# Optimization experiments

Hardware: AMD Instinct MI355X
Metric: run time of the kernel (lower is better)

## Reference

```python
import jax, jax.numpy as jnp
import numpy as np

HC = 64                 # half_context
PAD = HC + 3            # padding_idx row of positional table
NEG = 1.0e12            # additive mask constant from the torch code


def setup_inputs() -> dict:
    key = jax.random.key(0)
    ks = jax.random.split(key, 7)
    B, S, D, C = 32, 2048, 1024, 256
    embeds = jax.random.normal(ks[0], (B, S, D), dtype=jnp.float32)
    embeds_mask = jnp.ones((B, S), dtype=jnp.float32)
    latent = jax.random.normal(ks[1], (C, D), dtype=jnp.float32)
    att_diag = jax.random.normal(ks[2], (D,), dtype=jnp.float32)
    tok_diag = jax.random.normal(ks[3], (D,), dtype=jnp.float32)
    pos_table = jax.random.normal(ks[4], (2 * HC + 4, D), dtype=jnp.float32)
    pos_table = pos_table.at[PAD].set(0.0)  # padding_idx row is zeros
    tok_mult = jnp.ones((1,), dtype=jnp.float32)
    rel_pos_ids = jax.random.randint(ks[5], (B, S), 0, HC + 4, dtype=jnp.int32)
    return {
        "embeds": embeds,
        "embeds_mask": embeds_mask,
        "latent": latent,
        "att_diag": att_diag,
        "tok_diag": tok_diag,
        "pos_table": pos_table,
        "tok_mult": tok_mult,
        "rel_pos_ids": rel_pos_ids,
    }


def reference(embeds, embeds_mask, latent, att_diag, tok_diag, pos_table, tok_mult, rel_pos_ids):
    # positional-embedding gather and merge (dropouts are identity in eval)
    absolute_pos = rel_pos_ids + HC                       # [B,S]
    pos_embeds = pos_table[absolute_pos]                  # [B,S,D]
    merged = tok_mult[0] * embeds + pos_embeds            # [B,S,D]
    # entity-token attention scores: (latent * diag) @ merged^T
    scores = jnp.einsum('cd,bsd->bcs', latent * att_diag, merged)  # [B,C,S]
    m = embeds_mask[:, None, :]                           # [B,1,S]
    scores = scores * m + (m - 1.0) * NEG                 # mask-add
    top = jnp.max(scores, axis=1)                         # max over classes -> [B,S]
    att_probs = jax.nn.softmax(top, axis=1)               # softmax over tokens
    # weighted sum of (embeds * tok_diag) by attention probs -> [B,D]
    ctx_vecs = jnp.einsum('bsd,d,bs->bd', embeds, tok_diag, att_probs)
    return ctx_vecs
```

## Files before the change

### kernel.cpp

```cpp
#include <hip/hip_runtime.h>
#include <hip/hip_bf16.h>


#define HC 64
#define NEGV 1000000000000.0f

constexpr int Bb = 32, Ss = 2048, Dd = 1024, Cc = 256;
constexpr int NKC = 32;
constexpr int CT = Cc / 16;
constexpr int NBLK = 16;

typedef _Float16 f16x8 __attribute__((ext_vector_type(8)));
typedef float    f32x4 __attribute__((ext_vector_type(4)));

__global__ __launch_bounds__(256) void k_prep_w(
    const float* __restrict__ latent, const float* __restrict__ att_diag,
    _Float16* __restrict__ whi)
{
    const int idx = blockIdx.x * 256 + threadIdx.x;
    const int c = idx >> 10, k = idx & 1023;
    const float wv = latent[idx] * att_diag[k];
    const int kc = k >> 5, g = (k >> 3) & 3, i = k & 7;
    const int lane = (c & 15) + 16 * g, ct = c >> 4;
    whi[(size_t)kc * 8192 + (size_t)ct * 512 + lane * 8 + i] = (_Float16)wv;
}

__global__ __launch_bounds__(256, 2) void k_scores_mfma(
    const float* __restrict__ embeds,
    const float* __restrict__ mask,
    const float* __restrict__ pos_table,
    const float* __restrict__ tok_mult,
    const int*   __restrict__ rel_ids,
    const _Float16* __restrict__ whi,
    float* __restrict__ partial,
    float* __restrict__ mblk,
    float* __restrict__ zblk)
{
    __shared__ _Float16 sbufW[2][8192];
    __shared__ float    sbufE[2][4096];
    __shared__ float l_sh[128];
    __shared__ float w_sh[128];
    __shared__ float red2[2], zred[2];

    const int t  = threadIdx.x;
    const int wv = t >> 6;
    const int l  = t & 63;
    const int lr = l & 15;
    const int lg = l >> 4;

    const int b   = blockIdx.x >> 4;
    const int blk = blockIdx.x & 15;
    const int s0  = blk * 128;

    const float tm = tok_mult[0];

    const float* prow[2];
    #pragma unroll
    for (int st = 0; st < 2; st++) {
        const int tok = s0 + wv * 32 + st * 16 + lr;
        prow[st] = pos_table + (size_t)(rel_ids[b * Ss + tok] + HC) * Dd;
    }

    f32x4 acc[CT][2];
    #pragma unroll
    for (int ct = 0; ct < CT; ct++)
        #pragma unroll
        for (int st = 0; st < 2; st++) acc[ct][st] = (f32x4){0.f, 0.f, 0.f, 0.f};

    f32x4 p0[2], p1[2];
    auto loadP = [&](int kc) {
        const int k0 = kc * 32 + lg * 8;
        #pragma unroll
        for (int st = 0; st < 2; st++) {
            p0[st] = *(const f32x4*)(prow[st] + k0);
            p1[st] = *(const f32x4*)(prow[st] + k0 + 4);
        }
    };

    auto stageW = [&](int kc, _Float16* dst) {
        const _Float16* src = whi + (size_t)kc * 8192;
        #pragma unroll
        for (int i = 0; i < 4; i++) {
            const int off = (i * 4 + wv) << 9;
            __builtin_amdgcn_global_load_lds(
                (const __attribute__((address_space(1))) void*)(src + off + l * 8),
                (__attribute__((address_space(3))) void*)(dst + off),
                16, 0, 0);
        }
    };

    auto stageE = [&](int kc, float* dst) {
        const float* ebase = embeds + ((size_t)b * Ss + s0) * Dd + kc * 32;
        #pragma unroll
        for (int i = 0; i < 4; i++) {
            const int jbase = i * 256 + wv * 64;
            const int j = jbase + l;
            const int row = j >> 3, u = j & 7;
            const float* src = ebase + (size_t)row * Dd + ((u ^ (row & 7)) << 2);
            __builtin_amdgcn_global_load_lds(
                (const __attribute__((address_space(1))) void*)src,
                (__attribute__((address_space(3))) void*)(dst + jbase * 4),
                16, 0, 0);
        }
    };

    stageW(0, sbufW[0]);
    stageE(0, sbufE[0]);
    loadP(0);
    asm volatile("s_waitcnt vmcnt(4)" ::: "memory");
    __builtin_amdgcn_s_barrier();

    int cur = 0;
    for (int kc = 0; kc < NKC; kc++) {
        if (kc + 1 < NKC) {
            stageW(kc + 1, sbufW[cur ^ 1]);
            stageE(kc + 1, sbufE[cur ^ 1]);
        }

        f16x8 bh[2], bl[2];
        {
            const float* es = sbufE[cur];
            #pragma unroll
            for (int st = 0; st < 2; st++) {
                const int row = wv * 32 + st * 16 + lr;
                const int sw  = row & 7;
                const f32x4 x0 = *(const f32x4*)(es + row * 32 + (((lg << 1)    ) ^ sw) * 4);
                const f32x4 x1 = *(const f32x4*)(es + row * 32 + (((lg << 1) | 1) ^ sw) * 4);
                float e[8], p[8];
                *(f32x4*)&e[0] = x0;     *(f32x4*)&e[4] = x1;
                *(f32x4*)&p[0] = p0[st]; *(f32x4*)&p[4] = p1[st];
                #pragma unroll
                for (int i = 0; i < 8; i++) {
                    const float x = fmaf(tm, e[i], p[i]);
                    const _Float16 h = (_Float16)x;
                    bh[st][i] = h;
                    bl[st][i] = (_Float16)(x - (float)h);
                }
            }
        }
        if (kc + 1 < NKC) loadP(kc + 1);

        const _Float16* base = sbufW[cur];
        #pragma unroll
        for (int ct = 0; ct < CT; ct++) {
            const f16x8 ah = *(const f16x8*)(base + ct * 512 + l * 8);
            #pragma unroll
            for (int st = 0; st < 2; st++) {
                acc[ct][st] = __builtin_amdgcn_mfma_f32_16x16x32_f16(ah, bh[st], acc[ct][st], 0, 0, 0);
                acc[ct][st] = __builtin_amdgcn_mfma_f32_16x16x32_f16(ah, bl[st], acc[ct][st], 0, 0, 0);
            }
        }
        if (kc + 1 < NKC) { asm volatile("s_waitcnt vmcnt(4)" ::: "memory"); }
        else              { asm volatile("s_waitcnt vmcnt(0)" ::: "memory"); }
        __builtin_amdgcn_s_barrier();
        cur ^= 1;
    }

    #pragma unroll
    for (int st = 0; st < 2; st++) {
        float mx = acc[0][st][0];
        #pragma unroll
        for (int ct = 0; ct < CT; ct++)
            #pragma unroll
            for (int r = 0; r < 4; r++) mx = fmaxf(mx, acc[ct][st][r]);
        mx = fmaxf(mx, __shfl_xor(mx, 16));
        mx = fmaxf(mx, __shfl_xor(mx, 32));
        if (lg == 0) {
            const int si = wv * 32 + st * 16 + lr;
            const int s  = s0 + si;
            const float mk = mask[b * Ss + s];
            l_sh[si] = mx * mk + (mk - 1.0f) * NEGV;
        }
    }
    __syncthreads();

    if (t < 128) {
        float v = l_sh[t];
        #pragma unroll
        for (int o = 32; o >= 1; o >>= 1) v = fmaxf(v, __shfl_xor(v, o));
        if ((t & 63) == 0) red2[t >> 6] = v;
    }
    __syncthreads();
    const float Mb = fmaxf(red2[0], red2[1]);
    if (t < 128) w_sh[t] = expf(l_sh[t] - Mb);
    __syncthreads();
    if (t < 128) {
        float z = w_sh[t];
        #pragma unroll
        for (int o = 32; o >= 1; o >>= 1) z += __shfl_xor(z, o);
        if ((t & 63) == 0) zred[t >> 6] = z;
    }
    __syncthreads();

    {
        const float* eb = embeds + ((size_t)b * Ss + s0) * Dd + t * 4;
        f32x4 ca = (f32x4){0.f, 0.f, 0.f, 0.f};
        #pragma unroll 8
        for (int s = 0; s < 128; s++) {
            const float wgt = w_sh[s];
            const f32x4 ev = *(const f32x4*)(eb + (size_t)s * Dd);
            ca[0] = fmaf(wgt, ev[0], ca[0]);
            ca[1] = fmaf(wgt, ev[1], ca[1]);
            ca[2] = fmaf(wgt, ev[2], ca[2]);
            ca[3] = fmaf(wgt, ev[3], ca[3]);
        }
        *(f32x4*)(partial + ((size_t)(b * NBLK + blk)) * Dd + t * 4) = ca;
        if (t == 0) {
            mblk[b * NBLK + blk] = Mb;
            zblk[b * NBLK + blk] = zred[0] + zred[1];
        }
    }
}

__global__ __launch_bounds__(256) void k_finish(
    const float* __restrict__ mblk, const float* __restrict__ zblk,
    const float* __restrict__ partial, const float* __restrict__ tok_diag,
    float* __restrict__ out)
{
    __shared__ float cf[NBLK];
    const int b  = blockIdx.x >> 2;
    const int dq = blockIdx.x & 3;
    const int t  = threadIdx.x;

    if (t < 64) {
        const float mv = (t < NBLK) ? mblk[b * NBLK + t] : -3.4e38f;
        float M = mv;
        #pragma unroll
        for (int o = 32; o >= 1; o >>= 1) M = fmaxf(M, __shfl_xor(M, o));
        const float zv = (t < NBLK) ? zblk[b * NBLK + t] * expf(mv - M) : 0.f;
        float Z = zv;
        #pragma unroll
        for (int o = 32; o >= 1; o >>= 1) Z += __shfl_xor(Z, o);
        if (t < NBLK) cf[t] = expf(mv - M) / Z;
    }
    __syncthreads();

    const int d = dq * 256 + t;
    float a = 0.f;
    #pragma unroll
    for (int j = 0; j < NBLK; j++)
        a = fmaf(cf[j], partial[((size_t)(b * NBLK + j)) * Dd + d], a);
    out[(size_t)b * Dd + d] = a * tok_diag[d];
}

extern "C" void kernel_launch(void* const* d_in, const int* in_sizes, int n_in,
                              void* d_out, int out_size, void* d_ws, size_t ws_size,
                              hipStream_t stream) {
    const float* embeds    = (const float*)d_in[0];
    const float* mask      = (const float*)d_in[1];
    const float* latent    = (const float*)d_in[2];
    const float* att_diag  = (const float*)d_in[3];
    const float* tok_diag  = (const float*)d_in[4];
    const float* pos_table = (const float*)d_in[5];
    const float* tok_mult  = (const float*)d_in[6];
    const int*   rel_ids   = (const int*)d_in[7];
    float* out = (float*)d_out;

    char* ws = (char*)d_ws;
    _Float16* whi    = (_Float16*)(ws);
    float*    partial= (float*)(ws + 524288);
    float*    mblk   = (float*)(ws + 2621440);
    float*    zblk   = (float*)(ws + 2623488);

    k_prep_w<<<(Cc * Dd) / 256, 256, 0, stream>>>(latent, att_diag, whi);
    k_scores_mfma<<<Bb * NBLK, 256, 0, stream>>>(
        embeds, mask, pos_table, tok_mult, rel_ids, whi, partial, mblk, zblk);
    k_finish<<<Bb * 4, 256, 0, stream>>>(mblk, zblk, partial, tok_diag, out);
}
```

Measured before the change: 113.6 us.

## Precompute W·pos_table scores table and add after MFMA instead of gathering positions

Uses linearity of the score to split W·(tm·e + p) into (tm·W)·e plus a precomputed W·p table over all 132 positional rows, built by a new small kernel. The main MFMA kernel no longer gathers a positional row per token per K-chunk and no longer does the fused multiply-add before the f16 split, which removes per-iteration global gathers and VGPR pressure. Instead it adds a 256-entry row from the table to the accumulators before the max. tok_mult is folded into the f16 weights, which changes rounding slightly. The waitcnt is also tightened to vmcnt(0) because the P loads are gone.

```diff
diff --git a/kernel.cpp b/kernel.cpp
--- a/kernel.cpp
+++ b/kernel.cpp
@@ -15,23 +15,51 @@
 
 __global__ __launch_bounds__(256) void k_prep_w(
     const float* __restrict__ latent, const float* __restrict__ att_diag,
-    _Float16* __restrict__ whi)
+    const float* __restrict__ tok_mult, _Float16* __restrict__ whi)
 {
     const int idx = blockIdx.x * 256 + threadIdx.x;
     const int c = idx >> 10, k = idx & 1023;
-    const float wv = latent[idx] * att_diag[k];
+    const float wv = tok_mult[0] * latent[idx] * att_diag[k];
     const int kc = k >> 5, g = (k >> 3) & 3, i = k & 7;
     const int lane = (c & 15) + 16 * g, ct = c >> 4;
     whi[(size_t)kc * 8192 + (size_t)ct * 512 + lane * 8 + i] = (_Float16)wv;
 }
 
+__global__ __launch_bounds__(256) void k_wp(
+    const float* __restrict__ latent, const float* __restrict__ att_diag,
+    const float* __restrict__ pos_table, float* __restrict__ wpt)
+{
+    const int t   = threadIdx.x;
+    const int wv  = t >> 6, l = t & 63;
+    const int pid = blockIdx.x >> 6;
+    const int c   = (blockIdx.x & 63) * 4 + wv;
+
+    const float* lrow = latent    + (size_t)c   * Dd + l * 16;
+    const float* arow = att_diag  +                     l * 16;
+    const float* prow = pos_table + (size_t)pid * Dd + l * 16;
+
+    float s = 0.f;
+    #pragma unroll
+    for (int q = 0; q < 4; q++) {
+        const f32x4 lv = *(const f32x4*)(lrow + q * 4);
+        const f32x4 av = *(const f32x4*)(arow + q * 4);
+        const f32x4 pv = *(const f32x4*)(prow + q * 4);
+        s = fmaf(lv[0] * av[0], pv[0], s);
+        s = fmaf(lv[1] * av[1], pv[1], s);
+        s = fmaf(lv[2] * av[2], pv[2], s);
+        s = fmaf(lv[3] * av[3], pv[3], s);
+    }
+    #pragma unroll
+    for (int o = 32; o >= 1; o >>= 1) s += __shfl_xor(s, o);
+    if (l == 0) wpt[pid * Cc + c] = s;
+}
+
 __global__ __launch_bounds__(256, 2) void k_scores_mfma(
     const float* __restrict__ embeds,
     const float* __restrict__ mask,
-    const float* __restrict__ pos_table,
-    const float* __restrict__ tok_mult,
     const int*   __restrict__ rel_ids,
     const _Float16* __restrict__ whi,
+    const float* __restrict__ wpt,
     float* __restrict__ partial,
     float* __restrict__ mblk,
     float* __restrict__ zblk)
@@ -52,13 +80,11 @@
     const int blk = blockIdx.x & 15;
     const int s0  = blk * 128;
 
-    const float tm = tok_mult[0];
-
-    const float* prow[2];
+    int pid[2];
     #pragma unroll
     for (int st = 0; st < 2; st++) {
         const int tok = s0 + wv * 32 + st * 16 + lr;
-        prow[st] = pos_table + (size_t)(rel_ids[b * Ss + tok] + HC) * Dd;
+        pid[st] = rel_ids[b * Ss + tok] + HC;
     }
 
     f32x4 acc[CT][2];
@@ -66,16 +92,6 @@
     for (int ct = 0; ct < CT; ct++)
         #pragma unroll
         for (int st = 0; st < 2; st++) acc[ct][st] = (f32x4){0.f, 0.f, 0.f, 0.f};
-
-    f32x4 p0[2], p1[2];
-    auto loadP = [&](int kc) {
-        const int k0 = kc * 32 + lg * 8;
-        #pragma unroll
-        for (int st = 0; st < 2; st++) {
-            p0[st] = *(const f32x4*)(prow[st] + k0);
-            p1[st] = *(const f32x4*)(prow[st] + k0 + 4);
-        }
-    };
 
     auto stageW = [&](int kc, _Float16* dst) {
         const _Float16* src = whi + (size_t)kc * 8192;
@@ -106,8 +122,7 @@
 
     stageW(0, sbufW[0]);
     stageE(0, sbufE[0]);
-    loadP(0);
-    asm volatile("s_waitcnt vmcnt(4)" ::: "memory");
+    asm volatile("s_waitcnt vmcnt(0)" ::: "memory");
     __builtin_amdgcn_s_barrier();
 
     int cur = 0;
@@ -126,19 +141,16 @@
                 const int sw  = row & 7;
                 const f32x4 x0 = *(const f32x4*)(es + row * 32 + (((lg << 1)    ) ^ sw) * 4);
                 const f32x4 x1 = *(const f32x4*)(es + row * 32 + (((lg << 1) | 1) ^ sw) * 4);
-                float e[8], p[8];
-                *(f32x4*)&e[0] = x0;     *(f32x4*)&e[4] = x1;
-                *(f32x4*)&p[0] = p0[st]; *(f32x4*)&p[4] = p1[st];
+                float e[8];
+                *(f32x4*)&e[0] = x0; *(f32x4*)&e[4] = x1;
                 #pragma unroll
                 for (int i = 0; i < 8; i++) {
-                    const float x = fmaf(tm, e[i], p[i]);
-                    const _Float16 h = (_Float16)x;
+                    const _Float16 h = (_Float16)e[i];
                     bh[st][i] = h;
-                    bl[st][i] = (_Float16)(x - (float)h);
+                    bl[st][i] = (_Float16)(e[i] - (float)h);
                 }
             }
         }
-        if (kc + 1 < NKC) loadP(kc + 1);
 
         const _Float16* base = sbufW[cur];
         #pragma unroll
@@ -150,19 +162,21 @@
                 acc[ct][st] = __builtin_amdgcn_mfma_f32_16x16x32_f16(ah, bl[st], acc[ct][st], 0, 0, 0);
             }
         }
-        if (kc + 1 < NKC) { asm volatile("s_waitcnt vmcnt(4)" ::: "memory"); }
-        else              { asm volatile("s_waitcnt vmcnt(0)" ::: "memory"); }
+        asm volatile("s_waitcnt vmcnt(0)" ::: "memory");
         __builtin_amdgcn_s_barrier();
         cur ^= 1;
     }
 
     #pragma unroll
     for (int st = 0; st < 2; st++) {
-        float mx = acc[0][st][0];
-        #pragma unroll
-        for (int ct = 0; ct < CT; ct++)
+        const float* wrow = wpt + pid[st] * Cc + lg * 4;
+        float mx = -3.4e38f;
+        #pragma unroll
+        for (int ct = 0; ct < CT; ct++) {
+            const f32x4 wp = *(const f32x4*)(wrow + ct * 16);
             #pragma unroll
-            for (int r = 0; r < 4; r++) mx = fmaxf(mx, acc[ct][st][r]);
+            for (int r = 0; r < 4; r++) mx = fmaxf(mx, acc[ct][st][r] + wp[r]);
+        }
         mx = fmaxf(mx, __shfl_xor(mx, 16));
         mx = fmaxf(mx, __shfl_xor(mx, 32));
         if (lg == 0) {
@@ -258,12 +272,14 @@
 
     char* ws = (char*)d_ws;
     _Float16* whi    = (_Float16*)(ws);
-    float*    partial= (float*)(ws + 524288);
-    float*    mblk   = (float*)(ws + 2621440);
-    float*    zblk   = (float*)(ws + 2623488);
-
-    k_prep_w<<<(Cc * Dd) / 256, 256, 0, stream>>>(latent, att_diag, whi);
+    float*    wpt    = (float*)(ws + 524288);
+    float*    partial= (float*)(ws + 786432);
+    float*    mblk   = (float*)(ws + 2883584);
+    float*    zblk   = (float*)(ws + 2885632);
+
+    k_prep_w<<<(Cc * Dd) / 256, 256, 0, stream>>>(latent, att_diag, tok_mult, whi);
+    k_wp<<<132 * 64, 256, 0, stream>>>(latent, att_diag, pos_table, wpt);
     k_scores_mfma<<<Bb * NBLK, 256, 0, stream>>>(
-        embeds, mask, pos_table, tok_mult, rel_ids, whi, partial, mblk, zblk);
+        embeds, mask, rel_ids, whi, wpt, partial, mblk, zblk);
     k_finish<<<Bb * 4, 256, 0, stream>>>(mblk, zblk, partial, tok_diag, out);
 }
```

Result: slower. 135.5 us (+19.3%).
